# Kernel tuning notes

Hardware: AMD Instinct MI355X
Metric: run time of the kernel (lower is better)

Reference implementation:

```python
import jax, jax.numpy as jnp
import numpy as np


def _conv1x1(x, W, b):
    # x: [b,c,h,w], W: [out,in], b: [out]
    return jnp.einsum('oi,bihw->bohw', W, x) + b[None, :, None, None]


def setup_inputs() -> dict:
    key = jax.random.key(0)
    ks = jax.random.split(key, 8)
    B, C, H, W = 4, 256, 64, 64
    s = 1.0 / np.sqrt(C)
    return {
        'x1': jax.random.normal(ks[0], (B, C, H, W), jnp.float32),
        'x2': jax.random.normal(ks[1], (B, C, H, W), jnp.float32),
        'Wq': jax.random.normal(ks[2], (C, C), jnp.float32) * s,
        'bq': jax.random.normal(ks[3], (C,), jnp.float32) * 0.01,
        'Wk': jax.random.normal(ks[4], (C, C), jnp.float32) * s,
        'bk': jax.random.normal(ks[5], (C,), jnp.float32) * 0.01,
        'Wv': jax.random.normal(ks[6], (C, C), jnp.float32) * s,
        'bv': jax.random.normal(ks[7], (C,), jnp.float32) * 0.01,
    }


def reference(x1, x2, Wq, bq, Wk, bk, Wv, bv):
    b, c, h, w = x1.shape
    n = h * w
    q = _conv1x1(x1, Wq, bq).reshape(b, c, n)   # [b,c,n]
    k = _conv1x1(x2, Wk, bk).reshape(b, c, n)   # [b,c,n]
    v = _conv1x1(x2, Wv, bv).reshape(b, c, n)   # [b,c,n]
    # scores[b,i,j] = sum_c q[b,c,i] * k[b,c,j]; softmax over j (last dim)
    scores = jnp.einsum('bci,bcj->bij', q, k)
    attn = jax.nn.softmax(scores, axis=-1)      # [b,n,n]
    # out[b,c,i] = sum_j v[b,c,j] * attn[b,i,j]  (v @ attn^T)
    out = jnp.einsum('bcj,bij->bci', v, attn)
    return out.reshape(b, c, h, w)
```

## Files before the change

kernel.cpp:

```cpp
#include <hip/hip_runtime.h>

#define BATCH 4
#define CDIM 256
#define NDIM 4096
#define SPLITS 4
#define KSPLIT (NDIM / SPLITS)
#define JT 32
#define NTILES (KSPLIT / JT)

typedef unsigned short u16;
typedef unsigned int u32;
typedef _Float16 f16;
typedef __attribute__((ext_vector_type(8))) _Float16 half8;
typedef __attribute__((ext_vector_type(4))) float floatx4;

__device__ __forceinline__ void load_lds_128(const void* g, void* l) {
  __builtin_amdgcn_global_load_lds(
      (const __attribute__((address_space(1))) u32*)g,
      (__attribute__((address_space(3))) u32*)l, 16, 0, 0);
}

__global__ __launch_bounds__(256) void prep_w_k(
    const float* __restrict__ wq, const float* __restrict__ wk,
    const float* __restrict__ wv, f16* __restrict__ whq,
    f16* __restrict__ whk, f16* __restrict__ whv) {
  const int gid = blockIdx.x * 256 + threadIdx.x;
  const int a = gid >> 13;
  const int r = gid & 8191;
  const float* src = (a == 0) ? wq : ((a == 1) ? wk : wv);
  f16* dst = (a == 0) ? whq : ((a == 1) ? whk : whv);
  float4 v0 = *(const float4*)(src + r * 8);
  float4 v1 = *(const float4*)(src + r * 8 + 4);
  half8 h;
  h[0] = (f16)v0.x; h[1] = (f16)v0.y; h[2] = (f16)v0.z; h[3] = (f16)v0.w;
  h[4] = (f16)v1.x; h[5] = (f16)v1.y; h[6] = (f16)v1.z; h[7] = (f16)v1.w;
  *(half8*)(dst + r * 8) = h;
}

__global__ __launch_bounds__(256) void transpose_k(
    const float* __restrict__ x1, const float* __restrict__ x2,
    f16* __restrict__ xt1, f16* __restrict__ xt2) {
  __shared__ __align__(16) float tile[64 * 68];
  const int z = blockIdx.z;
  const float* src = (z & 1) ? x2 : x1;
  f16* dst = (z & 1) ? xt2 : xt1;
  const int b = z >> 1;
  src += (size_t)b * CDIM * NDIM;
  dst += (size_t)b * NDIM * CDIM;
  const int n0 = blockIdx.x * 64, c0 = blockIdx.y * 64;
  const int t = threadIdx.x;
#pragma unroll
  for (int it = 0; it < 4; ++it) {
    int chunk = t + it * 256;
    int row = chunk >> 4;
    int col4 = (chunk & 15) << 2;
    float4 v = *(const float4*)(src + (size_t)(c0 + row) * NDIM + (n0 + col4));
    *(float4*)&tile[row * 68 + col4] = v;
  }
  __syncthreads();
#pragma unroll
  for (int it = 0; it < 2; ++it) {
    int task = t + it * 256;
    int nl = task >> 3;
    int cb = (task & 7) << 3;
    half8 h;
#pragma unroll
    for (int j = 0; j < 8; ++j) h[j] = (f16)tile[(cb + j) * 68 + nl];
    *(half8*)(dst + (size_t)(n0 + nl) * CDIM + (c0 + cb)) = h;
  }
}

__global__ __launch_bounds__(256, 2) void proj_qk_k(
    const f16* __restrict__ xt1, const f16* __restrict__ xt2,
    const f16* __restrict__ whq, const float* __restrict__ bq,
    const f16* __restrict__ whk, const float* __restrict__ bk,
    f16* __restrict__ qt, f16* __restrict__ kt) {
  const int z = blockIdx.z;
  const int which = z & 1, b = z >> 1;
  const f16* xt = which ? xt2 : xt1;
  const f16* w = which ? whk : whq;
  const float* bias = which ? bk : bq;
  f16* outp = which ? kt : qt;
  xt += (size_t)b * NDIM * CDIM;
  outp += (size_t)b * NDIM * CDIM;
  const int c0 = blockIdx.x * 128, i0 = blockIdx.y * 128;
  const int tid = threadIdx.x;
  const int wave = tid >> 6, lane = tid & 63, l16 = lane & 15, grp = lane >> 4;
  const int wi = (wave & 1) * 64, wc = (wave >> 1) * 64;
  floatx4 acc[4][4];
#pragma unroll
  for (int mb = 0; mb < 4; ++mb)
#pragma unroll
    for (int nb = 0; nb < 4; ++nb) acc[mb][nb] = (floatx4){0.f, 0.f, 0.f, 0.f};
#pragma unroll
  for (int ks = 0; ks < 8; ++ks) {
    const int kofs = ks * 32 + grp * 8;
    half8 a[4], bb[4];
#pragma unroll
    for (int mb = 0; mb < 4; ++mb)
      a[mb] = *(const half8*)(xt + (size_t)(i0 + wi + mb * 16 + l16) * CDIM + kofs);
#pragma unroll
    for (int nb = 0; nb < 4; ++nb)
      bb[nb] = *(const half8*)(w + (size_t)(c0 + wc + nb * 16 + l16) * CDIM + kofs);
#pragma unroll
    for (int mb = 0; mb < 4; ++mb)
#pragma unroll
      for (int nb = 0; nb < 4; ++nb)
        acc[mb][nb] = __builtin_amdgcn_mfma_f32_16x16x32_f16(a[mb], bb[nb], acc[mb][nb], 0, 0, 0);
  }
#pragma unroll
  for (int nb = 0; nb < 4; ++nb) {
    const int c = c0 + wc + nb * 16 + l16;
    const float bv = bias[c];
#pragma unroll
    for (int mb = 0; mb < 4; ++mb) {
      const int ibase = i0 + wi + mb * 16 + grp * 4;
#pragma unroll
      for (int r = 0; r < 4; ++r)
        outp[(size_t)(ibase + r) * CDIM + c] = (f16)(acc[mb][nb][r] + bv);
    }
  }
}

__global__ __launch_bounds__(256, 2) void proj_v_k(
    const f16* __restrict__ xt2, const f16* __restrict__ whv,
    const float* __restrict__ bv, f16* __restrict__ vsout) {
  const int b = blockIdx.z;
  const f16* xt = xt2 + (size_t)b * NDIM * CDIM;
  f16* outp = vsout + (size_t)b * CDIM * NDIM;
  const int c0 = blockIdx.x * 128, j0 = blockIdx.y * 128;
  const int tid = threadIdx.x;
  const int wave = tid >> 6, lane = tid & 63, l16 = lane & 15, grp = lane >> 4;
  const int wc = (wave & 1) * 64, wj = (wave >> 1) * 64;
  floatx4 acc[4][4];
#pragma unroll
  for (int mb = 0; mb < 4; ++mb)
#pragma unroll
    for (int nb = 0; nb < 4; ++nb) acc[mb][nb] = (floatx4){0.f, 0.f, 0.f, 0.f};
#pragma unroll
  for (int ks = 0; ks < 8; ++ks) {
    const int kofs = ks * 32 + grp * 8;
    half8 a[4], bb[4];
#pragma unroll
    for (int mb = 0; mb < 4; ++mb)
      a[mb] = *(const half8*)(whv + (size_t)(c0 + wc + mb * 16 + l16) * CDIM + kofs);
#pragma unroll
    for (int nb = 0; nb < 4; ++nb)
      bb[nb] = *(const half8*)(xt + (size_t)(j0 + wj + nb * 16 + l16) * CDIM + kofs);
#pragma unroll
    for (int mb = 0; mb < 4; ++mb)
#pragma unroll
      for (int nb = 0; nb < 4; ++nb)
        acc[mb][nb] = __builtin_amdgcn_mfma_f32_16x16x32_f16(a[mb], bb[nb], acc[mb][nb], 0, 0, 0);
  }
#pragma unroll
  for (int mb = 0; mb < 4; ++mb)
#pragma unroll
    for (int r = 0; r < 4; ++r) {
      const int c = c0 + wc + mb * 16 + grp * 4 + r;
      const float bvv = bv[c];
#pragma unroll
      for (int nb = 0; nb < 4; ++nb) {
        const int j = j0 + wj + nb * 16 + l16;
        outp[(size_t)c * NDIM + j] = (f16)(acc[mb][nb][r] + bvv);
      }
    }
}

__global__ __launch_bounds__(256, 2) void flash_k(
    const f16* __restrict__ qt, const f16* __restrict__ kt,
    const f16* __restrict__ vs, f16* __restrict__ pO,
    float* __restrict__ pm, float* __restrict__ pl) {
  __shared__ __align__(16) u16 smem[32768 + 4608];
  const int bx = blockIdx.x;
  const int c16 = bx & 15;
  const int b = c16 >> 2, s = c16 & 3;
  const int i0 = (bx >> 4) * 128;
  const int jwin = s * KSPLIT;
  const f16* Q = qt + (size_t)b * NDIM * CDIM;
  const f16* K = kt + (size_t)b * NDIM * CDIM;
  const f16* V = vs + (size_t)b * CDIM * NDIM;
  const int tid = threadIdx.x;
  const int wave = tid >> 6, lane = tid & 63, l16 = lane & 15, grp = lane >> 4;
  float* Pw = (float*)(smem + 32768) + wave * (16 * 36);

  half8 qf[2][8];
#pragma unroll
  for (int mb = 0; mb < 2; ++mb)
#pragma unroll
    for (int ks = 0; ks < 8; ++ks)
      qf[mb][ks] = *(const half8*)(Q + (size_t)(i0 + wave * 32 + mb * 16 + l16) * CDIM +
                                   ks * 32 + grp * 8);

  floatx4 O[2][16];
#pragma unroll
  for (int mb = 0; mb < 2; ++mb)
#pragma unroll
    for (int cb = 0; cb < 16; ++cb) O[mb][cb] = (floatx4){0.f, 0.f, 0.f, 0.f};
  float m_[2] = {-1e30f, -1e30f};
  float lsum[2] = {0.f, 0.f};

  const int kr2 = lane >> 5, kp = lane & 31;
  const int vrow = lane >> 2, vp = lane & 3;

#define STAGE(J0, BUF)                                                         \
  {                                                                            \
    u16* sK = smem + (BUF) * 16384;                                            \
    u16* sV = sK + 8192;                                                       \
    _Pragma("unroll") for (int it = 0; it < 4; ++it) {                         \
      const int row = wave * 8 + it * 2 + kr2;                                 \
      const int g = kp ^ (row & 7);                                            \
      load_lds_128(K + (size_t)((J0) + row) * CDIM + g * 8,                    \
                   &sK[(wave * 8 + it * 2) * 256]);                            \
    }                                                                          \
    _Pragma("unroll") for (int it = 0; it < 4; ++it) {                         \
      const int c = wave * 64 + it * 16 + vrow;                                \
      const int g = vp ^ ((c >> 2) & 3);                                       \
      load_lds_128(V + (size_t)c * NDIM + (J0) + g * 8,                        \
                   &sV[(wave * 64 + it * 16) * 32]);                           \
    }                                                                          \
  }

  STAGE(jwin, 0)

  for (int tt = 0; tt < NTILES; ++tt) {
    __syncthreads();
    if (tt + 1 < NTILES) STAGE(jwin + (tt + 1) * JT, (tt + 1) & 1)
    u16* bK = smem + (tt & 1) * 16384;
    u16* bV = bK + 8192;

    floatx4 S[2][2];
#pragma unroll
    for (int mb = 0; mb < 2; ++mb)
#pragma unroll
      for (int jb = 0; jb < 2; ++jb) S[mb][jb] = (floatx4){0.f, 0.f, 0.f, 0.f};
#pragma unroll
    for (int ks = 0; ks < 8; ++ks) {
      const int chunk = ks * 4 + grp;
#pragma unroll
      for (int jb = 0; jb < 2; ++jb) {
        const int row = jb * 16 + l16;
        half8 kf = *(const half8*)&bK[row * 256 + ((chunk ^ (row & 7)) << 3)];
        S[0][jb] = __builtin_amdgcn_mfma_f32_16x16x32_f16(qf[0][ks], kf, S[0][jb], 0, 0, 0);
        S[1][jb] = __builtin_amdgcn_mfma_f32_16x16x32_f16(qf[1][ks], kf, S[1][jb], 0, 0, 0);
      }
    }

    float alpha[2];
    half8 pa[2];
#pragma unroll
    for (int mb = 0; mb < 2; ++mb) {
#pragma unroll
      for (int jb = 0; jb < 2; ++jb)
#pragma unroll
        for (int r = 0; r < 4; ++r)
          Pw[(grp * 4 + r) * 36 + jb * 16 + l16] = S[mb][jb][r];
      floatx4 u0 = *(const floatx4*)&Pw[l16 * 36 + grp * 8];
      floatx4 u1 = *(const floatx4*)&Pw[l16 * 36 + grp * 8 + 4];
      float mx = fmaxf(fmaxf(fmaxf(u0[0], u0[1]), fmaxf(u0[2], u0[3])),
                       fmaxf(fmaxf(u1[0], u1[1]), fmaxf(u1[2], u1[3])));
      mx = fmaxf(mx, __shfl_xor(mx, 16, 64));
      mx = fmaxf(mx, __shfl_xor(mx, 32, 64));
      const float mnew = fmaxf(m_[mb], mx);
      alpha[mb] = __expf(m_[mb] - mnew);
      m_[mb] = mnew;
      float pe[8];
#pragma unroll
      for (int j = 0; j < 4; ++j) pe[j] = __expf(u0[j] - mnew);
#pragma unroll
      for (int j = 0; j < 4; ++j) pe[4 + j] = __expf(u1[j] - mnew);
      const float ps = ((pe[0] + pe[1]) + (pe[2] + pe[3])) +
                       ((pe[4] + pe[5]) + (pe[6] + pe[7]));
      lsum[mb] = lsum[mb] * alpha[mb] + ps;
      half8 h;
#pragma unroll
      for (int j = 0; j < 8; ++j) h[j] = (f16)pe[j];
      pa[mb] = h;
    }

    if (__any(alpha[0] < 1.f) || __any(alpha[1] < 1.f)) {
#pragma unroll
      for (int mb = 0; mb < 2; ++mb)
#pragma unroll
        for (int cb = 0; cb < 16; ++cb) O[mb][cb] *= alpha[mb];
    }

#pragma unroll
    for (int cb = 0; cb < 16; ++cb) {
      const int c = cb * 16 + l16;
      half8 vf = *(const half8*)&bV[c * 32 + ((grp ^ ((c >> 2) & 3)) << 3)];
      O[0][cb] = __builtin_amdgcn_mfma_f32_16x16x32_f16(vf, pa[0], O[0][cb], 0, 0, 0);
      O[1][cb] = __builtin_amdgcn_mfma_f32_16x16x32_f16(vf, pa[1], O[1][cb], 0, 0, 0);
    }
  }

#pragma unroll
  for (int mb = 0; mb < 2; ++mb) {
    lsum[mb] += __shfl_xor(lsum[mb], 16, 64);
    lsum[mb] += __shfl_xor(lsum[mb], 32, 64);
  }
  if (grp == 0) {
    const int base = (b * SPLITS + s) * NDIM + i0;
#pragma unroll
    for (int mb = 0; mb < 2; ++mb) {
      const int i = wave * 32 + mb * 16 + l16;
      pm[base + i] = m_[mb];
      pl[base + i] = lsum[mb];
    }
  }

  const size_t pbase = (size_t)(b * SPLITS + s) * CDIM * NDIM;
#pragma unroll
  for (int mb = 0; mb < 2; ++mb) {
    const int i = i0 + wave * 32 + mb * 16 + l16;
#pragma unroll
    for (int cb = 0; cb < 16; ++cb) {
      const int c = cb * 16 + grp * 4;
#pragma unroll
      for (int r = 0; r < 4; ++r)
        pO[pbase + (size_t)(c + r) * NDIM + i] = (f16)O[mb][cb][r];
    }
  }
}

__global__ __launch_bounds__(256) void combine_k(
    const f16* __restrict__ pO, const float* __restrict__ pm,
    const float* __restrict__ pl, float* __restrict__ out) {
  __shared__ float su[SPLITS][64];
  const int b = blockIdx.x >> 6;
  const int i0 = (blockIdx.x & 63) * 64;
  const int t = threadIdx.x;
  if (t < 64) {
    const int i = i0 + t;
    float mv[SPLITS], w[SPLITS];
    float M = -3e38f;
#pragma unroll
    for (int s = 0; s < SPLITS; ++s) {
      mv[s] = pm[(b * SPLITS + s) * NDIM + i];
      M = fmaxf(M, mv[s]);
    }
    float L = 0.f;
#pragma unroll
    for (int s = 0; s < SPLITS; ++s) {
      w[s] = __expf(mv[s] - M);
      L += pl[(b * SPLITS + s) * NDIM + i] * w[s];
    }
    const float invL = 1.0f / L;
#pragma unroll
    for (int s = 0; s < SPLITS; ++s) su[s][t] = w[s] * invL;
  }
  __syncthreads();
#pragma unroll
  for (int it = 0; it < 8; ++it) {
    const int task = t + it * 256;
    const int c = task >> 3, p = (task & 7) * 8;
    float acc[8] = {0.f, 0.f, 0.f, 0.f, 0.f, 0.f, 0.f, 0.f};
#pragma unroll
    for (int s = 0; s < SPLITS; ++s) {
      const f16* src = pO + ((size_t)(b * SPLITS + s) * CDIM + c) * NDIM + i0 + p;
      half8 h = *(const half8*)src;
#pragma unroll
      for (int j = 0; j < 8; ++j) acc[j] += su[s][p + j] * (float)h[j];
    }
    float* dst = out + ((size_t)b * CDIM + c) * NDIM + i0 + p;
    float4 lo = {acc[0], acc[1], acc[2], acc[3]};
    float4 hi = {acc[4], acc[5], acc[6], acc[7]};
    *(float4*)dst = lo;
    *(float4*)(dst + 4) = hi;
  }
}

extern "C" void kernel_launch(void* const* d_in, const int* in_sizes, int n_in,
                              void* d_out, int out_size, void* d_ws, size_t ws_size,
                              hipStream_t stream) {
  const float* x1 = (const float*)d_in[0];
  const float* x2 = (const float*)d_in[1];
  const float* Wq = (const float*)d_in[2];
  const float* bq = (const float*)d_in[3];
  const float* Wk = (const float*)d_in[4];
  const float* bk = (const float*)d_in[5];
  const float* Wv = (const float*)d_in[6];
  const float* bv = (const float*)d_in[7];
  float* out = (float*)d_out;
  char* ws = (char*)d_ws;
  f16* qtp = (f16*)(ws + 0);
  f16* ktp = (f16*)(ws + 8388608);
  f16* vsp = (f16*)(ws + 16777216);
  f16* xt1 = (f16*)(ws + 25165824);
  f16* xt2 = (f16*)(ws + 33554432);
  f16* whq = (f16*)(ws + 41943040);
  f16* whk = whq + CDIM * CDIM;
  f16* whv = whk + CDIM * CDIM;
  f16* pO = (f16*)(ws + 25165824);
  float* pm = (float*)(ws + 58720256);
  float* pl = (float*)(ws + 58982400);

  prep_w_k<<<dim3(96), dim3(256), 0, stream>>>(Wq, Wk, Wv, whq, whk, whv);
  transpose_k<<<dim3(NDIM / 64, CDIM / 64, 2 * BATCH), dim3(256), 0, stream>>>(x1, x2, xt1, xt2);
  proj_qk_k<<<dim3(2, 32, 2 * BATCH), dim3(256), 0, stream>>>(xt1, xt2, whq, bq, whk, bk, qtp, ktp);
  proj_v_k<<<dim3(2, 32, BATCH), dim3(256), 0, stream>>>(xt2, whv, bv, vsp);
  flash_k<<<dim3(512), dim3(256), 0, stream>>>(qtp, ktp, vsp, pO, pm, pl);
  combine_k<<<dim3(256), dim3(256), 0, stream>>>(pO, pm, pl, out);
}
```

Before: 261.9 us.

## Fuse input transpose and QKV projections into one kernel; store scores as fp16

Replaces the separate transpose, Q/K projection and V projection kernels with one kernel that loads a tile of x, converts it to fp16 in shared memory, and computes the projection from there. This removes the global round trip for transposed activations and two launches. The flash kernel also writes the score tile to LDS in fp16 instead of fp32, halving that scratch space and its traffic. Risks include strided scalar LDS reads in the fused projection and reduced precision of scores before the softmax.

```diff
diff --git a/kernel.cpp b/kernel.cpp
--- a/kernel.cpp
+++ b/kernel.cpp
@@ -37,141 +37,119 @@
   *(half8*)(dst + r * 8) = h;
 }
 
-__global__ __launch_bounds__(256) void transpose_k(
+__global__ __launch_bounds__(256, 2) void proj_fused_k(
     const float* __restrict__ x1, const float* __restrict__ x2,
-    f16* __restrict__ xt1, f16* __restrict__ xt2) {
-  __shared__ __align__(16) float tile[64 * 68];
-  const int z = blockIdx.z;
-  const float* src = (z & 1) ? x2 : x1;
-  f16* dst = (z & 1) ? xt2 : xt1;
-  const int b = z >> 1;
-  src += (size_t)b * CDIM * NDIM;
-  dst += (size_t)b * NDIM * CDIM;
-  const int n0 = blockIdx.x * 64, c0 = blockIdx.y * 64;
-  const int t = threadIdx.x;
-#pragma unroll
-  for (int it = 0; it < 4; ++it) {
-    int chunk = t + it * 256;
-    int row = chunk >> 4;
-    int col4 = (chunk & 15) << 2;
-    float4 v = *(const float4*)(src + (size_t)(c0 + row) * NDIM + (n0 + col4));
-    *(float4*)&tile[row * 68 + col4] = v;
-  }
-  __syncthreads();
-#pragma unroll
-  for (int it = 0; it < 2; ++it) {
-    int task = t + it * 256;
-    int nl = task >> 3;
-    int cb = (task & 7) << 3;
-    half8 h;
-#pragma unroll
-    for (int j = 0; j < 8; ++j) h[j] = (f16)tile[(cb + j) * 68 + nl];
-    *(half8*)(dst + (size_t)(n0 + nl) * CDIM + (c0 + cb)) = h;
-  }
-}
-
-__global__ __launch_bounds__(256, 2) void proj_qk_k(
-    const f16* __restrict__ xt1, const f16* __restrict__ xt2,
     const f16* __restrict__ whq, const float* __restrict__ bq,
     const f16* __restrict__ whk, const float* __restrict__ bk,
-    f16* __restrict__ qt, f16* __restrict__ kt) {
-  const int z = blockIdx.z;
-  const int which = z & 1, b = z >> 1;
-  const f16* xt = which ? xt2 : xt1;
-  const f16* w = which ? whk : whq;
-  const float* bias = which ? bk : bq;
-  f16* outp = which ? kt : qt;
-  xt += (size_t)b * NDIM * CDIM;
-  outp += (size_t)b * NDIM * CDIM;
-  const int c0 = blockIdx.x * 128, i0 = blockIdx.y * 128;
-  const int tid = threadIdx.x;
-  const int wave = tid >> 6, lane = tid & 63, l16 = lane & 15, grp = lane >> 4;
-  const int wi = (wave & 1) * 64, wc = (wave >> 1) * 64;
-  floatx4 acc[4][4];
-#pragma unroll
-  for (int mb = 0; mb < 4; ++mb)
-#pragma unroll
-    for (int nb = 0; nb < 4; ++nb) acc[mb][nb] = (floatx4){0.f, 0.f, 0.f, 0.f};
-#pragma unroll
-  for (int ks = 0; ks < 8; ++ks) {
-    const int kofs = ks * 32 + grp * 8;
-    half8 a[4], bb[4];
-#pragma unroll
-    for (int mb = 0; mb < 4; ++mb)
-      a[mb] = *(const half8*)(xt + (size_t)(i0 + wi + mb * 16 + l16) * CDIM + kofs);
-#pragma unroll
-    for (int nb = 0; nb < 4; ++nb)
-      bb[nb] = *(const half8*)(w + (size_t)(c0 + wc + nb * 16 + l16) * CDIM + kofs);
-#pragma unroll
-    for (int mb = 0; mb < 4; ++mb)
-#pragma unroll
-      for (int nb = 0; nb < 4; ++nb)
-        acc[mb][nb] = __builtin_amdgcn_mfma_f32_16x16x32_f16(a[mb], bb[nb], acc[mb][nb], 0, 0, 0);
-  }
-#pragma unroll
-  for (int nb = 0; nb < 4; ++nb) {
-    const int c = c0 + wc + nb * 16 + l16;
-    const float bv = bias[c];
-#pragma unroll
-    for (int mb = 0; mb < 4; ++mb) {
-      const int ibase = i0 + wi + mb * 16 + grp * 4;
-#pragma unroll
-      for (int r = 0; r < 4; ++r)
-        outp[(size_t)(ibase + r) * CDIM + c] = (f16)(acc[mb][nb][r] + bv);
-    }
-  }
-}
-
-__global__ __launch_bounds__(256, 2) void proj_v_k(
-    const f16* __restrict__ xt2, const f16* __restrict__ whv,
-    const float* __restrict__ bv, f16* __restrict__ vsout) {
-  const int b = blockIdx.z;
-  const f16* xt = xt2 + (size_t)b * NDIM * CDIM;
-  f16* outp = vsout + (size_t)b * CDIM * NDIM;
-  const int c0 = blockIdx.x * 128, j0 = blockIdx.y * 128;
-  const int tid = threadIdx.x;
-  const int wave = tid >> 6, lane = tid & 63, l16 = lane & 15, grp = lane >> 4;
-  const int wc = (wave & 1) * 64, wj = (wave >> 1) * 64;
-  floatx4 acc[4][4];
-#pragma unroll
-  for (int mb = 0; mb < 4; ++mb)
-#pragma unroll
-    for (int nb = 0; nb < 4; ++nb) acc[mb][nb] = (floatx4){0.f, 0.f, 0.f, 0.f};
-#pragma unroll
-  for (int ks = 0; ks < 8; ++ks) {
-    const int kofs = ks * 32 + grp * 8;
-    half8 a[4], bb[4];
-#pragma unroll
-    for (int mb = 0; mb < 4; ++mb)
-      a[mb] = *(const half8*)(whv + (size_t)(c0 + wc + mb * 16 + l16) * CDIM + kofs);
-#pragma unroll
-    for (int nb = 0; nb < 4; ++nb)
-      bb[nb] = *(const half8*)(xt + (size_t)(j0 + wj + nb * 16 + l16) * CDIM + kofs);
-#pragma unroll
-    for (int mb = 0; mb < 4; ++mb)
-#pragma unroll
-      for (int nb = 0; nb < 4; ++nb)
-        acc[mb][nb] = __builtin_amdgcn_mfma_f32_16x16x32_f16(a[mb], bb[nb], acc[mb][nb], 0, 0, 0);
-  }
-#pragma unroll
-  for (int mb = 0; mb < 4; ++mb)
-#pragma unroll
-    for (int r = 0; r < 4; ++r) {
-      const int c = c0 + wc + mb * 16 + grp * 4 + r;
-      const float bvv = bv[c];
+    const f16* __restrict__ whv, const float* __restrict__ bv,
+    f16* __restrict__ qt, f16* __restrict__ kt, f16* __restrict__ vsp) {
+  __shared__ __align__(16) u16 xt[256 * 132];
+  const int j0 = blockIdx.x * 128;
+  const int b = blockIdx.y;
+  const int proj = blockIdx.z;
+  const float* xs = ((proj == 0) ? x1 : x2) + (size_t)b * CDIM * NDIM;
+  const int t = threadIdx.x;
+#pragma unroll
+  for (int it = 0; it < 32; ++it) {
+    const int flat = t + it * 256;
+    const int c = flat >> 5;
+    const int n4 = (flat & 31) << 2;
+    float4 v = *(const float4*)(xs + (size_t)c * NDIM + j0 + n4);
+    union { f16 h[4]; uint2 u; } pk;
+    pk.h[0] = (f16)v.x; pk.h[1] = (f16)v.y; pk.h[2] = (f16)v.z; pk.h[3] = (f16)v.w;
+    *(uint2*)&xt[c * 132 + n4] = pk.u;
+  }
+  __syncthreads();
+  const int wave = t >> 6, lane = t & 63, l16 = lane & 15, grp = lane >> 4;
+  const f16* xth = (const f16*)xt;
+
+  if (proj < 2) {
+    const f16* w = proj ? whk : whq;
+    const float* bias = proj ? bk : bq;
+    f16* outp = (proj ? kt : qt) + (size_t)b * NDIM * CDIM;
+    floatx4 acc[2][16];
+#pragma unroll
+    for (int mb = 0; mb < 2; ++mb)
+#pragma unroll
+      for (int nb = 0; nb < 16; ++nb) acc[mb][nb] = (floatx4){0.f, 0.f, 0.f, 0.f};
+#pragma unroll
+    for (int ks = 0; ks < 8; ++ks) {
+      half8 a[2];
+#pragma unroll
+      for (int mb = 0; mb < 2; ++mb) {
+        const int n = wave * 32 + mb * 16 + l16;
+        half8 av;
+#pragma unroll
+        for (int jj = 0; jj < 8; ++jj)
+          av[jj] = xth[(ks * 32 + grp * 8 + jj) * 132 + n];
+        a[mb] = av;
+      }
+#pragma unroll
+      for (int nb = 0; nb < 16; ++nb) {
+        half8 bb = *(const half8*)(w + (size_t)(nb * 16 + l16) * CDIM + ks * 32 + grp * 8);
+        acc[0][nb] = __builtin_amdgcn_mfma_f32_16x16x32_f16(a[0], bb, acc[0][nb], 0, 0, 0);
+        acc[1][nb] = __builtin_amdgcn_mfma_f32_16x16x32_f16(a[1], bb, acc[1][nb], 0, 0, 0);
+      }
+    }
+#pragma unroll
+    for (int nb = 0; nb < 16; ++nb) {
+      const int c = nb * 16 + l16;
+      const float bvv = bias[c];
+#pragma unroll
+      for (int mb = 0; mb < 2; ++mb) {
+        const int jbase = j0 + wave * 32 + mb * 16 + grp * 4;
+#pragma unroll
+        for (int r = 0; r < 4; ++r)
+          outp[(size_t)(jbase + r) * CDIM + c] = (f16)(acc[mb][nb][r] + bvv);
+      }
+    }
+  } else {
+    f16* outp = vsp + (size_t)b * CDIM * NDIM;
+    const int cw = (wave & 1) * 128;
+    const int jw = (wave >> 1) * 64;
+    floatx4 acc[8][4];
+#pragma unroll
+    for (int mb = 0; mb < 8; ++mb)
+#pragma unroll
+      for (int nb = 0; nb < 4; ++nb) acc[mb][nb] = (floatx4){0.f, 0.f, 0.f, 0.f};
+#pragma unroll
+    for (int ks = 0; ks < 8; ++ks) {
+      half8 a[8];
+#pragma unroll
+      for (int mb = 0; mb < 8; ++mb)
+        a[mb] = *(const half8*)(whv + (size_t)(cw + mb * 16 + l16) * CDIM + ks * 32 + grp * 8);
 #pragma unroll
       for (int nb = 0; nb < 4; ++nb) {
-        const int j = j0 + wj + nb * 16 + l16;
-        outp[(size_t)c * NDIM + j] = (f16)(acc[mb][nb][r] + bvv);
-      }
-    }
+        const int n = jw + nb * 16 + l16;
+        half8 bv8;
+#pragma unroll
+        for (int jj = 0; jj < 8; ++jj)
+          bv8[jj] = xth[(ks * 32 + grp * 8 + jj) * 132 + n];
+#pragma unroll
+        for (int mb = 0; mb < 8; ++mb)
+          acc[mb][nb] = __builtin_amdgcn_mfma_f32_16x16x32_f16(a[mb], bv8, acc[mb][nb], 0, 0, 0);
+      }
+    }
+#pragma unroll
+    for (int mb = 0; mb < 8; ++mb)
+#pragma unroll
+      for (int r = 0; r < 4; ++r) {
+        const int c = cw + mb * 16 + grp * 4 + r;
+        const float bvv = bv[c];
+#pragma unroll
+        for (int nb = 0; nb < 4; ++nb) {
+          const int j = j0 + jw + nb * 16 + l16;
+          outp[(size_t)c * NDIM + j] = (f16)(acc[mb][nb][r] + bvv);
+        }
+      }
+  }
 }
 
 __global__ __launch_bounds__(256, 2) void flash_k(
     const f16* __restrict__ qt, const f16* __restrict__ kt,
     const f16* __restrict__ vs, f16* __restrict__ pO,
     float* __restrict__ pm, float* __restrict__ pl) {
-  __shared__ __align__(16) u16 smem[32768 + 4608];
+  __shared__ __align__(16) u16 smem[32768 + 2560];
   const int bx = blockIdx.x;
   const int c16 = bx & 15;
   const int b = c16 >> 2, s = c16 & 3;
@@ -182,7 +160,7 @@
   const f16* V = vs + (size_t)b * CDIM * NDIM;
   const int tid = threadIdx.x;
   const int wave = tid >> 6, lane = tid & 63, l16 = lane & 15, grp = lane >> 4;
-  float* Pw = (float*)(smem + 32768) + wave * (16 * 36);
+  f16* Pw = (f16*)(smem + 32768) + wave * (16 * 40);
 
   half8 qf[2][8];
 #pragma unroll
@@ -254,11 +232,13 @@
       for (int jb = 0; jb < 2; ++jb)
 #pragma unroll
         for (int r = 0; r < 4; ++r)
-          Pw[(grp * 4 + r) * 36 + jb * 16 + l16] = S[mb][jb][r];
-      floatx4 u0 = *(const floatx4*)&Pw[l16 * 36 + grp * 8];
-      floatx4 u1 = *(const floatx4*)&Pw[l16 * 36 + grp * 8 + 4];
-      float mx = fmaxf(fmaxf(fmaxf(u0[0], u0[1]), fmaxf(u0[2], u0[3])),
-                       fmaxf(fmaxf(u1[0], u1[1]), fmaxf(u1[2], u1[3])));
+          Pw[(grp * 4 + r) * 40 + jb * 16 + l16] = (f16)S[mb][jb][r];
+      half8 rawh = *(const half8*)&Pw[l16 * 40 + grp * 8];
+      float u[8];
+#pragma unroll
+      for (int j = 0; j < 8; ++j) u[j] = (float)rawh[j];
+      float mx = fmaxf(fmaxf(fmaxf(u[0], u[1]), fmaxf(u[2], u[3])),
+                       fmaxf(fmaxf(u[4], u[5]), fmaxf(u[6], u[7])));
       mx = fmaxf(mx, __shfl_xor(mx, 16, 64));
       mx = fmaxf(mx, __shfl_xor(mx, 32, 64));
       const float mnew = fmaxf(m_[mb], mx);
@@ -266,9 +246,7 @@
       m_[mb] = mnew;
       float pe[8];
 #pragma unroll
-      for (int j = 0; j < 4; ++j) pe[j] = __expf(u0[j] - mnew);
-#pragma unroll
-      for (int j = 0; j < 4; ++j) pe[4 + j] = __expf(u1[j] - mnew);
+      for (int j = 0; j < 8; ++j) pe[j] = __expf(u[j] - mnew);
       const float ps = ((pe[0] + pe[1]) + (pe[2] + pe[3])) +
                        ((pe[4] + pe[5]) + (pe[6] + pe[7]));
       lsum[mb] = lsum[mb] * alpha[mb] + ps;
@@ -386,8 +364,6 @@
   f16* qtp = (f16*)(ws + 0);
   f16* ktp = (f16*)(ws + 8388608);
   f16* vsp = (f16*)(ws + 16777216);
-  f16* xt1 = (f16*)(ws + 25165824);
-  f16* xt2 = (f16*)(ws + 33554432);
   f16* whq = (f16*)(ws + 41943040);
   f16* whk = whq + CDIM * CDIM;
   f16* whv = whk + CDIM * CDIM;
@@ -396,9 +372,8 @@
   float* pl = (float*)(ws + 58982400);
 
   prep_w_k<<<dim3(96), dim3(256), 0, stream>>>(Wq, Wk, Wv, whq, whk, whv);
-  transpose_k<<<dim3(NDIM / 64, CDIM / 64, 2 * BATCH), dim3(256), 0, stream>>>(x1, x2, xt1, xt2);
-  proj_qk_k<<<dim3(2, 32, 2 * BATCH), dim3(256), 0, stream>>>(xt1, xt2, whq, bq, whk, bk, qtp, ktp);
-  proj_v_k<<<dim3(2, 32, BATCH), dim3(256), 0, stream>>>(xt2, whv, bv, vsp);
+  proj_fused_k<<<dim3(NDIM / 128, BATCH, 3), dim3(256), 0, stream>>>(
+      x1, x2, whq, bq, whk, bk, whv, bv, qtp, ktp, vsp);
   flash_k<<<dim3(512), dim3(256), 0, stream>>>(qtp, ktp, vsp, pO, pm, pl);
   combine_k<<<dim3(256), dim3(256), 0, stream>>>(pO, pm, pl, out);
 }
```

New measurement: 254.4 us. 2.9% less time.
